# Optimization experiments

Measured on AMD Instinct MI355X. Metric: run time of the kernel, lower is better.

Reference implementation:

```python
import jax, jax.numpy as jnp
import numpy as np

B, C, V, L = 32, 32, 207, 128
C_OUT = 32
ORDER = 2


def setup_inputs() -> dict:
    key = jax.random.key(0)
    ks = jax.random.split(key, 6)
    x = jax.random.normal(ks[0], (B, C, V, L), dtype=jnp.float32)
    A0 = jax.random.uniform(ks[1], (V, V), dtype=jnp.float32) / V
    A1 = jax.random.uniform(ks[2], (V, V), dtype=jnp.float32) / V
    A2 = jax.random.uniform(ks[3], (V, V), dtype=jnp.float32) / V
    c_in_total = (ORDER * 3 + 1) * C  # 224
    W = jax.random.normal(ks[4], (C_OUT, c_in_total), dtype=jnp.float32) * 0.05
    b = jax.random.normal(ks[5], (C_OUT,), dtype=jnp.float32) * 0.05
    return {"x": x, "A0": A0, "A1": A1, "A2": A2, "W": W, "b": b}


def _nconv(x, A):
    # x: [n, c, v, l], A: [v, w] -> [n, c, w, l]
    return jnp.einsum('ncvl,vw->ncwl', x, A)


def reference(x, A0, A1, A2, W, b):
    outs = [x]
    for A in (A0, A1, A2):
        x1 = _nconv(x, A)
        outs.append(x1)
        for _ in range(2, ORDER + 1):
            x1 = _nconv(x1, A)
            outs.append(x1)
    h = jnp.concatenate(outs, axis=1)  # [n, 7*C, v, l]
    # 1x1 Conv2d == channel-mixing matmul; dropout is identity in eval mode
    return jnp.einsum('ncvl,oc->novl', h, W) + b[None, :, None, None]
```

## Files before the change

### kernel.cpp

```cpp
#include <hip/hip_runtime.h>

#define VDIM 207
#define LDIM 128
#define VP 224
#define VL (VDIM*LDIM)
#define NC 1024
#define NPOINT (32*VL)
#define APITCH 232
#define SWZ(row, colb) ((row) * 464 + ((colb) ^ (((row) & 1) << 5)))

typedef unsigned short u16;
typedef unsigned int u32;
typedef __attribute__((ext_vector_type(4))) float f32x4;
typedef __attribute__((ext_vector_type(8))) short s16x8;

__device__ __forceinline__ u16 f2bf(float f) {
  u32 u = __float_as_uint(f);
  return (u16)((u + 0x7FFFu + ((u >> 16) & 1u)) >> 16);
}
__device__ __forceinline__ float bf2f(u16 h) {
  return __uint_as_float(((u32)h) << 16);
}

__global__ void k_prep(const float* __restrict__ A0, const float* __restrict__ A1,
                       const float* __restrict__ A2, const float* __restrict__ W,
                       u16* __restrict__ MT, float* __restrict__ WT,
                       u16* __restrict__ Wb) {
  int idx = blockIdx.x * 256 + threadIdx.x;
  if (idx < 3 * VP * VP) {
    int i = idx / (VP * VP);
    int r = idx % (VP * VP);
    int w = r / VP, v = r % VP;
    const float* A = (i == 0) ? A0 : ((i == 1) ? A1 : A2);
    float f = (w < VDIM && v < VDIM) ? A[v * VDIM + w] : 0.f;
    MT[(size_t)(2 * i) * (VP * VP) + r] = f2bf(f);
  } else {
    int j = idx - 3 * VP * VP;
    if (j < VP * 32) {
      int k = j >> 5, o = j & 31;
      WT[j] = W[o * 224 + k];
    } else if (j < 2 * VP * 32) {
      int j2 = j - VP * 32;
      Wb[j2] = f2bf(W[j2]);
    }
  }
}

__global__ void k_sq(const float* __restrict__ A0, const float* __restrict__ A1,
                     const float* __restrict__ A2, u16* __restrict__ MT) {
  int idx = blockIdx.x * 256 + threadIdx.x;
  if (idx >= 3 * VP * VP) return;
  int i = idx / (VP * VP), r = idx % (VP * VP);
  int w = r / VP, v = r % VP;
  const float* A = (i == 0) ? A0 : ((i == 1) ? A1 : A2);
  float s = 0.f;
  if (w < VDIM && v < VDIM) {
#pragma unroll 4
    for (int u = 0; u < VDIM; ++u) s += A[v * VDIM + u] * A[u * VDIM + w];
  }
  MT[(size_t)(2 * i + 1) * (VP * VP) + r] = f2bf(s);
}

__global__ __launch_bounds__(256) void k_xt(const float* __restrict__ x,
                                            u16* __restrict__ xT) {
  __shared__ float tile[64 * 130];
  int nc = blockIdx.x;
  const float* xs = x + (size_t)nc * VL;
  u16* xd = xT + (size_t)nc * (128 * VP);
  int tid = threadIdx.x;
  for (int ch = 0; ch < 4; ++ch) {
    int v0 = ch * 64;
    __syncthreads();
#pragma unroll
    for (int j = 0; j < 8; ++j) {
      int idx = j * 256 + tid;
      int vr = idx >> 5, c4 = idx & 31;
      int v = v0 + vr;
      float4 val = make_float4(0.f, 0.f, 0.f, 0.f);
      if (v < VDIM) val = *(const float4*)(xs + (size_t)v * LDIM + c4 * 4);
      float* trow = &tile[vr * 130 + c4 * 4];
      *(float2*)(trow) = make_float2(val.x, val.y);
      *(float2*)(trow + 2) = make_float2(val.z, val.w);
    }
    __syncthreads();
    int l = tid >> 1, h = tid & 1;
    int vbase = v0 + h * 32;
    if (vbase < VP) {
      u32 wd[16];
#pragma unroll
      for (int j = 0; j < 16; ++j) {
        int v = vbase + 2 * j;
        float f0 = (v < VDIM) ? tile[(h * 32 + 2 * j) * 130 + l] : 0.f;
        float f1 = (v + 1 < VDIM) ? tile[(h * 32 + 2 * j + 1) * 130 + l] : 0.f;
        wd[j] = (u32)f2bf(f0) | ((u32)f2bf(f1) << 16);
      }
      uint4* dst = (uint4*)(xd + (size_t)l * VP + vbase);
#pragma unroll
      for (int t = 0; t < 4; ++t)
        dst[t] = make_uint4(wd[4 * t], wd[4 * t + 1], wd[4 * t + 2], wd[4 * t + 3]);
    }
  }
}

template <int NMT>
__global__ __launch_bounds__(256, 4) void k_gemm(const u16* __restrict__ xT,
                                                 const u16* __restrict__ MT,
                                                 u16* __restrict__ zbuf,
                                                 int j0, int jcount) {
  __shared__ __align__(16) u16 A_s[NMT * 16 * APITCH];
  int tid = threadIdx.x;
  int lane = tid & 63, wn = tid >> 6;
  int lane15 = lane & 15, lgrp = lane >> 4;
  int bid = blockIdx.x;
  int nc, rowbase;
  if (NMT == 5) { nc = bid; rowbase = 0; }
  else { nc = bid >> 1; rowbase = 80 + 64 * (bid & 1); }
  const u16* xg = xT + (size_t)nc * (128 * VP);
  int col0 = wn * 32 + lane15, col1 = col0 + 16;

  s16x8 bx0[7], bx1[7];
#pragma unroll
  for (int ks = 0; ks < 7; ++ks) {
    bx0[ks] = *(const s16x8*)(xg + (size_t)col0 * VP + ks * 32 + lgrp * 8);
    bx1[ks] = *(const s16x8*)(xg + (size_t)col1 * VP + ks * 32 + lgrp * 8);
  }

  for (int jj = 0; jj < jcount; ++jj) {
    const u16* Mg = MT + (size_t)(j0 + jj) * (VP * VP) + (size_t)rowbase * VP;
    for (int t = tid; t < NMT * 16 * 28; t += 256) {
      int r = t / 28, cq = t - r * 28;
      *(uint4*)((char*)A_s + SWZ(r, cq * 16)) = *(const uint4*)(Mg + r * VP + cq * 8);
    }
    __syncthreads();

    f32x4 acc[NMT][2];
#pragma unroll
    for (int m = 0; m < NMT; ++m) {
      acc[m][0] = (f32x4){0.f, 0.f, 0.f, 0.f};
      acc[m][1] = (f32x4){0.f, 0.f, 0.f, 0.f};
    }
    for (int ks = 0; ks < 7; ++ks) {
      int colb = ks * 64 + lgrp * 16;
#pragma unroll
      for (int mt = 0; mt < NMT; ++mt) {
        s16x8 af = *(const s16x8*)((char*)A_s + SWZ(mt * 16 + lane15, colb));
        asm("v_mfma_f32_16x16x32_bf16 %0, %1, %2, %0"
            : "+v"(acc[mt][0]) : "v"(af), "v"(bx0[ks]));
        asm("v_mfma_f32_16x16x32_bf16 %0, %1, %2, %0"
            : "+v"(acc[mt][1]) : "v"(af), "v"(bx1[ks]));
      }
    }
    __syncthreads();

    u16* zg = zbuf + (size_t)jj * ((size_t)NC * VL) + (size_t)nc * VL;
#pragma unroll
    for (int mt = 0; mt < NMT; ++mt) {
#pragma unroll
      for (int nt = 0; nt < 2; ++nt) {
        f32x4 a = acc[mt][nt];
        int col = wn * 32 + nt * 16 + lane15;
        int wb = rowbase + mt * 16 + lgrp * 4;
        u16 u0 = f2bf(a.x), u1 = f2bf(a.y), u2 = f2bf(a.z), u3 = f2bf(a.w);
        if (wb + 0 < VDIM) zg[(wb + 0) * LDIM + col] = u0;
        if (wb + 1 < VDIM) zg[(wb + 1) * LDIM + col] = u1;
        if (wb + 2 < VDIM) zg[(wb + 2) * LDIM + col] = u2;
        if (wb + 3 < VDIM) zg[(wb + 3) * LDIM + col] = u3;
      }
    }
  }
}

__global__ __launch_bounds__(512, 4) void k_mixm(const float* __restrict__ x,
                                                 const u16* __restrict__ zb,
                                                 const u16* __restrict__ Wb,
                                                 const float* __restrict__ bias,
                                                 float* __restrict__ out) {
  __shared__ __align__(16) u16 hT_s[128 * APITCH];
  __shared__ __align__(16) u16 tile[2][32 * 136];
  int tid = threadIdx.x;
  int bid = blockIdx.x;
  int n = bid / 207, pt = bid - n * 207;
  int p0 = pt * 128;
  int lane = tid & 63, wn = tid >> 6;
  int lane15 = lane & 15, lgrp = lane >> 4;

  s16x8 wa0[7], wa1[7];
#pragma unroll
  for (int ks = 0; ks < 7; ++ks) {
    wa0[ks] = *(const s16x8*)(Wb + lane15 * 224 + ks * 32 + lgrp * 8);
    wa1[ks] = *(const s16x8*)(Wb + (16 + lane15) * 224 + ks * 32 + lgrp * 8);
  }

#pragma unroll
  for (int t = 0; t < 2; ++t) {
    int j = t * 512 + tid;
    int c = j >> 5, q = j & 31;
    float4 v = *(const float4*)(x + (size_t)(n * 32 + c) * VL + p0 + q * 4);
    int sc = 2 * ((c >> 3) & 3);
    u16* tp = tile[0] + c * 136;
    *(u32*)(tp + ((q * 4) ^ sc)) = (u32)f2bf(v.x) | ((u32)f2bf(v.y) << 16);
    *(u32*)(tp + ((q * 4 + 2) ^ sc)) = (u32)f2bf(v.z) | ((u32)f2bf(v.w) << 16);
  }
  __syncthreads();

  int cur = 0;
  int zc = tid >> 4, zq = tid & 15;
  for (int g7 = 0; g7 < 7; ++g7) {
    uint4 zv;
    if (g7 < 6)
      zv = *(const uint4*)(zb + ((size_t)(g7 << 10) + n * 32 + zc) * VL + p0 + zq * 8);
#pragma unroll
    for (int t = 0; t < 4; ++t) {
      int j = t * 512 + tid;
      int cp = j & 15, p = j >> 4;
      int sc = 2 * ((cp >> 2) & 3);
      const u16* tp = tile[cur];
      u32 w = (u32)tp[(2 * cp) * 136 + (p ^ sc)] |
              ((u32)tp[(2 * cp + 1) * 136 + (p ^ sc)] << 16);
      *(u32*)(hT_s + p * APITCH + g7 * 32 + 2 * cp) = w;
    }
    if (g7 < 6) {
      int sc = 2 * ((zc >> 3) & 3);
      u16* tp = tile[cur ^ 1] + zc * 136;
      u32 zd[4] = {zv.x, zv.y, zv.z, zv.w};
#pragma unroll
      for (int t = 0; t < 4; ++t)
        *(u32*)(tp + ((zq * 8 + 2 * t) ^ sc)) = zd[t];
    }
    __syncthreads();
    cur ^= 1;
  }

  f32x4 acc[2];
  acc[0] = (f32x4){0.f, 0.f, 0.f, 0.f};
  acc[1] = (f32x4){0.f, 0.f, 0.f, 0.f};
  int colp = wn * 16 + lane15;
#pragma unroll
  for (int ks = 0; ks < 7; ++ks) {
    s16x8 bfrag = *(const s16x8*)(hT_s + colp * APITCH + ks * 32 + lgrp * 8);
    asm("v_mfma_f32_16x16x32_bf16 %0, %1, %2, %0"
        : "+v"(acc[0]) : "v"(wa0[ks]), "v"(bfrag));
    asm("v_mfma_f32_16x16x32_bf16 %0, %1, %2, %0"
        : "+v"(acc[1]) : "v"(wa1[ks]), "v"(bfrag));
  }

#pragma unroll
  for (int mt = 0; mt < 2; ++mt) {
#pragma unroll
    for (int j = 0; j < 4; ++j) {
      int o = mt * 16 + lgrp * 4 + j;
      out[(size_t)(n * 32 + o) * VL + p0 + colp] = acc[mt][j] + bias[o];
    }
  }
}

template <int MODE, int NZ>
__global__ __launch_bounds__(256, 4) void k_mix(const float* __restrict__ x,
                                                const u16* __restrict__ zb,
                                                const float* __restrict__ WT,
                                                const float* __restrict__ bias,
                                                float* __restrict__ out, int wk0) {
  int t = blockIdx.x * 256 + threadIdx.x;
  int pp = t * 2;
  int n = pp / VL;
  int rem = pp - n * VL;
  float* op = out + (size_t)n * 32 * VL + rem;
  f32x4 a0[8], a1[8];

  if (MODE == 0) {
#pragma unroll
    for (int j = 0; j < 8; ++j) {
      f32x4 bv = *(const f32x4*)(bias + 4 * j);
      a0[j] = bv;
      a1[j] = bv;
    }
    const float* xp = x + (size_t)n * 32 * VL + rem;
#pragma unroll
    for (int c0 = 0; c0 < 32; c0 += 4) {
      float2 v[4];
#pragma unroll
      for (int q = 0; q < 4; ++q)
        v[q] = *(const float2*)(xp + (size_t)(c0 + q) * VL);
#pragma unroll
      for (int q = 0; q < 4; ++q) {
        const float* wv = WT + (c0 + q) * 32;
#pragma unroll
        for (int j = 0; j < 8; ++j) {
          f32x4 w4 = *(const f32x4*)(wv + 4 * j);
          a0[j] += w4 * v[q].x;
          a1[j] += w4 * v[q].y;
        }
      }
    }
  } else {
#pragma unroll
    for (int j = 0; j < 8; ++j) {
#pragma unroll
      for (int q = 0; q < 4; ++q) {
        float2 r = *(const float2*)(op + (size_t)(4 * j + q) * VL);
        a0[j][q] = r.x;
        a1[j][q] = r.y;
      }
    }
  }

#pragma unroll 1
  for (int g = 0; g < NZ; ++g) {
    const u16* zp = zb + ((size_t)g * NC + (size_t)n * 32) * VL + rem;
    const float* wg = WT + (wk0 + g * 32) * 32;
#pragma unroll
    for (int c0 = 0; c0 < 32; c0 += 4) {
      u32 zv[4];
#pragma unroll
      for (int q = 0; q < 4; ++q)
        zv[q] = *(const u32*)(zp + (size_t)(c0 + q) * VL);
#pragma unroll
      for (int q = 0; q < 4; ++q) {
        float f0 = bf2f((u16)(zv[q] & 0xFFFFu));
        float f1 = bf2f((u16)(zv[q] >> 16));
        const float* wv = wg + (c0 + q) * 32;
#pragma unroll
        for (int j = 0; j < 8; ++j) {
          f32x4 w4 = *(const f32x4*)(wv + 4 * j);
          a0[j] += w4 * f0;
          a1[j] += w4 * f1;
        }
      }
    }
  }

#pragma unroll
  for (int j = 0; j < 8; ++j) {
#pragma unroll
    for (int q = 0; q < 4; ++q) {
      float2 r;
      r.x = a0[j][q];
      r.y = a1[j][q];
      *(float2*)(op + (size_t)(4 * j + q) * VL) = r;
    }
  }
}

extern "C" void kernel_launch(void* const* d_in, const int* in_sizes, int n_in,
                              void* d_out, int out_size, void* d_ws, size_t ws_size,
                              hipStream_t stream) {
  const float* x = (const float*)d_in[0];
  const float* A0 = (const float*)d_in[1];
  const float* A1 = (const float*)d_in[2];
  const float* A2 = (const float*)d_in[3];
  const float* W = (const float*)d_in[4];
  const float* b = (const float*)d_in[5];
  float* out = (float*)d_out;

  const size_t xT_sz = (size_t)NC * 128 * VP * 2;
  const size_t MT_sz = (size_t)6 * VP * VP * 2;
  const size_t WT_sz = (size_t)VP * 32 * 4;
  const size_t Wb_sz = (size_t)VP * 32 * 2;
  const size_t slot_sz = (size_t)NC * VL * 2;

  char* wp = (char*)d_ws;
  u16* xT = (u16*)wp; wp += (xT_sz + 255) & ~(size_t)255;
  u16* MT = (u16*)wp; wp += (MT_sz + 255) & ~(size_t)255;
  float* WT = (float*)wp; wp += (WT_sz + 255) & ~(size_t)255;
  u16* Wb = (u16*)wp; wp += (Wb_sz + 255) & ~(size_t)255;
  u16* zbuf = (u16*)wp;
  size_t base = (size_t)(wp - (char*)d_ws);
  bool bigws = ws_size >= base + 6 * slot_sz;

  k_prep<<<644, 256, 0, stream>>>(A0, A1, A2, W, MT, WT, Wb);
  k_sq<<<588, 256, 0, stream>>>(A0, A1, A2, MT);
  k_xt<<<NC, 256, 0, stream>>>(x, xT);
  if (bigws) {
    k_gemm<5><<<NC, 256, 0, stream>>>(xT, MT, zbuf, 0, 6);
    k_gemm<4><<<2 * NC, 256, 0, stream>>>(xT, MT, zbuf, 0, 6);
    k_mixm<<<32 * 207, 512, 0, stream>>>(x, zbuf, Wb, b, out);
  } else {
    const int mixgrid = NPOINT / 512;
    k_mix<0, 0><<<mixgrid, 256, 0, stream>>>(x, nullptr, WT, b, out, 32);
    for (int i = 0; i < 3; ++i) {
      k_gemm<5><<<NC, 256, 0, stream>>>(xT, MT, zbuf, 2 * i, 2);
      k_gemm<4><<<2 * NC, 256, 0, stream>>>(xT, MT, zbuf, 2 * i, 2);
      k_mix<1, 2><<<mixgrid, 256, 0, stream>>>(nullptr, zbuf, WT, nullptr, out,
                                               (1 + 2 * i) * 32);
    }
  }
}
```

Measured before the change: 406.9 us.

## Merge split GEMM launches into one kernel looping over row chunks; prefetch z in mix

Replaces the two k_gemm launches (one block per nc for the first 80 rows, two blocks per nc for the rest) with a single k_gemm2 launch. Each block walks all 208 output rows in 64-row chunks, which removes a launch and reuses the x fragments held in registers across every row chunk instead of reloading them in three blocks. In exchange the grid has fewer blocks (1024), so each block does more serial work and latency hiding may drop. k_mixm is also changed to software-pipeline the z loads, issuing the next slice's global load before the current slice's shared-memory transpose.

After: 383.6 us. -5.7%, faster.

```diff
diff --git a/kernel.cpp b/kernel.cpp
--- a/kernel.cpp
+++ b/kernel.cpp
@@ -102,19 +102,15 @@
   }
 }
 
-template <int NMT>
-__global__ __launch_bounds__(256, 4) void k_gemm(const u16* __restrict__ xT,
-                                                 const u16* __restrict__ MT,
-                                                 u16* __restrict__ zbuf,
-                                                 int j0, int jcount) {
-  __shared__ __align__(16) u16 A_s[NMT * 16 * APITCH];
+__global__ __launch_bounds__(256, 4) void k_gemm2(const u16* __restrict__ xT,
+                                                  const u16* __restrict__ MT,
+                                                  u16* __restrict__ zbuf,
+                                                  int j0, int jcount) {
+  __shared__ __align__(16) u16 A_s[64 * APITCH];
   int tid = threadIdx.x;
   int lane = tid & 63, wn = tid >> 6;
   int lane15 = lane & 15, lgrp = lane >> 4;
-  int bid = blockIdx.x;
-  int nc, rowbase;
-  if (NMT == 5) { nc = bid; rowbase = 0; }
-  else { nc = bid >> 1; rowbase = 80 + 64 * (bid & 1); }
+  int nc = blockIdx.x;
   const u16* xg = xT + (size_t)nc * (128 * VP);
   int col0 = wn * 32 + lane15, col1 = col0 + 16;
 
@@ -125,46 +121,55 @@
     bx1[ks] = *(const s16x8*)(xg + (size_t)col1 * VP + ks * 32 + lgrp * 8);
   }
 
-  for (int jj = 0; jj < jcount; ++jj) {
-    const u16* Mg = MT + (size_t)(j0 + jj) * (VP * VP) + (size_t)rowbase * VP;
-    for (int t = tid; t < NMT * 16 * 28; t += 256) {
+  const int niter = jcount * 4;
+  for (int u = 0; u < niter; ++u) {
+    int j = u >> 2, ch = u & 3;
+    int rowbase = ch * 64;
+    int nrows = (ch < 3) ? 64 : 16;
+    const u16* Mg = MT + (size_t)(j0 + j) * (VP * VP) + (size_t)rowbase * VP;
+    for (int t = tid; t < nrows * 28; t += 256) {
       int r = t / 28, cq = t - r * 28;
       *(uint4*)((char*)A_s + SWZ(r, cq * 16)) = *(const uint4*)(Mg + r * VP + cq * 8);
     }
     __syncthreads();
 
-    f32x4 acc[NMT][2];
-#pragma unroll
-    for (int m = 0; m < NMT; ++m) {
+    int nmt = (ch < 3) ? 4 : 1;
+    f32x4 acc[4][2];
+#pragma unroll
+    for (int m = 0; m < 4; ++m) {
       acc[m][0] = (f32x4){0.f, 0.f, 0.f, 0.f};
       acc[m][1] = (f32x4){0.f, 0.f, 0.f, 0.f};
     }
     for (int ks = 0; ks < 7; ++ks) {
       int colb = ks * 64 + lgrp * 16;
 #pragma unroll
-      for (int mt = 0; mt < NMT; ++mt) {
-        s16x8 af = *(const s16x8*)((char*)A_s + SWZ(mt * 16 + lane15, colb));
-        asm("v_mfma_f32_16x16x32_bf16 %0, %1, %2, %0"
-            : "+v"(acc[mt][0]) : "v"(af), "v"(bx0[ks]));
-        asm("v_mfma_f32_16x16x32_bf16 %0, %1, %2, %0"
-            : "+v"(acc[mt][1]) : "v"(af), "v"(bx1[ks]));
-      }
-    }
-    __syncthreads();
-
-    u16* zg = zbuf + (size_t)jj * ((size_t)NC * VL) + (size_t)nc * VL;
-#pragma unroll
-    for (int mt = 0; mt < NMT; ++mt) {
-#pragma unroll
-      for (int nt = 0; nt < 2; ++nt) {
-        f32x4 a = acc[mt][nt];
-        int col = wn * 32 + nt * 16 + lane15;
-        int wb = rowbase + mt * 16 + lgrp * 4;
-        u16 u0 = f2bf(a.x), u1 = f2bf(a.y), u2 = f2bf(a.z), u3 = f2bf(a.w);
-        if (wb + 0 < VDIM) zg[(wb + 0) * LDIM + col] = u0;
-        if (wb + 1 < VDIM) zg[(wb + 1) * LDIM + col] = u1;
-        if (wb + 2 < VDIM) zg[(wb + 2) * LDIM + col] = u2;
-        if (wb + 3 < VDIM) zg[(wb + 3) * LDIM + col] = u3;
+      for (int mt = 0; mt < 4; ++mt) {
+        if (mt < nmt) {
+          s16x8 af = *(const s16x8*)((char*)A_s + SWZ(mt * 16 + lane15, colb));
+          asm("v_mfma_f32_16x16x32_bf16 %0, %1, %2, %0"
+              : "+v"(acc[mt][0]) : "v"(af), "v"(bx0[ks]));
+          asm("v_mfma_f32_16x16x32_bf16 %0, %1, %2, %0"
+              : "+v"(acc[mt][1]) : "v"(af), "v"(bx1[ks]));
+        }
+      }
+    }
+    __syncthreads();
+
+    u16* zg = zbuf + (size_t)j * ((size_t)NC * VL) + (size_t)nc * VL;
+#pragma unroll
+    for (int mt = 0; mt < 4; ++mt) {
+      if (mt < nmt) {
+#pragma unroll
+        for (int nt = 0; nt < 2; ++nt) {
+          f32x4 a = acc[mt][nt];
+          int col = wn * 32 + nt * 16 + lane15;
+          int wb = rowbase + mt * 16 + lgrp * 4;
+          u16 u0 = f2bf(a.x), u1 = f2bf(a.y), u2 = f2bf(a.z), u3 = f2bf(a.w);
+          if (wb + 0 < VDIM) zg[(wb + 0) * LDIM + col] = u0;
+          if (wb + 1 < VDIM) zg[(wb + 1) * LDIM + col] = u1;
+          if (wb + 2 < VDIM) zg[(wb + 2) * LDIM + col] = u2;
+          if (wb + 3 < VDIM) zg[(wb + 3) * LDIM + col] = u3;
+        }
       }
     }
   }
@@ -201,14 +206,15 @@
     *(u32*)(tp + ((q * 4) ^ sc)) = (u32)f2bf(v.x) | ((u32)f2bf(v.y) << 16);
     *(u32*)(tp + ((q * 4 + 2) ^ sc)) = (u32)f2bf(v.z) | ((u32)f2bf(v.w) << 16);
   }
+  int zc = tid >> 4, zq = tid & 15;
+  uint4 zvA = *(const uint4*)(zb + ((size_t)(n * 32) + zc) * VL + p0 + zq * 8);
   __syncthreads();
 
   int cur = 0;
-  int zc = tid >> 4, zq = tid & 15;
   for (int g7 = 0; g7 < 7; ++g7) {
-    uint4 zv;
-    if (g7 < 6)
-      zv = *(const uint4*)(zb + ((size_t)(g7 << 10) + n * 32 + zc) * VL + p0 + zq * 8);
+    uint4 zvB = zvA;
+    if (g7 < 5)
+      zvB = *(const uint4*)(zb + ((size_t)((g7 + 1) << 10) + n * 32 + zc) * VL + p0 + zq * 8);
 #pragma unroll
     for (int t = 0; t < 4; ++t) {
       int j = t * 512 + tid;
@@ -222,12 +228,13 @@
     if (g7 < 6) {
       int sc = 2 * ((zc >> 3) & 3);
       u16* tp = tile[cur ^ 1] + zc * 136;
-      u32 zd[4] = {zv.x, zv.y, zv.z, zv.w};
+      u32 zd[4] = {zvA.x, zvA.y, zvA.z, zvA.w};
 #pragma unroll
       for (int t = 0; t < 4; ++t)
         *(u32*)(tp + ((zq * 8 + 2 * t) ^ sc)) = zd[t];
     }
     __syncthreads();
+    zvA = zvB;
     cur ^= 1;
   }
 
@@ -371,15 +378,13 @@
   k_sq<<<588, 256, 0, stream>>>(A0, A1, A2, MT);
   k_xt<<<NC, 256, 0, stream>>>(x, xT);
   if (bigws) {
-    k_gemm<5><<<NC, 256, 0, stream>>>(xT, MT, zbuf, 0, 6);
-    k_gemm<4><<<2 * NC, 256, 0, stream>>>(xT, MT, zbuf, 0, 6);
+    k_gemm2<<<NC, 256, 0, stream>>>(xT, MT, zbuf, 0, 6);
     k_mixm<<<32 * 207, 512, 0, stream>>>(x, zbuf, Wb, b, out);
   } else {
     const int mixgrid = NPOINT / 512;
     k_mix<0, 0><<<mixgrid, 256, 0, stream>>>(x, nullptr, WT, b, out, 32);
     for (int i = 0; i < 3; ++i) {
-      k_gemm<5><<<NC, 256, 0, stream>>>(xT, MT, zbuf, 2 * i, 2);
-      k_gemm<4><<<2 * NC, 256, 0, stream>>>(xT, MT, zbuf, 2 * i, 2);
+      k_gemm2<<<NC, 256, 0, stream>>>(xT, MT, zbuf, 2 * i, 2);
       k_mix<1, 2><<<mixgrid, 256, 0, stream>>>(nullptr, zbuf, WT, nullptr, out,
                                                (1 + 2 * i) * 32);
     }
```
